# Kernel optimization log

Measured on AMD Instinct MI355X. Metric: run time of the kernel, lower is better.

Reference implementation:

```python
import jax, jax.numpy as jnp
import numpy as np

EPS = 1e-3       # module eps for mask normalization
LN_EPS = 1e-5    # torch LayerNorm default eps


def _layernorm(x, w, b):
    mu = jnp.mean(x, axis=-1, keepdims=True)
    var = jnp.var(x, axis=-1, keepdims=True)
    return (x - mu) * jax.lax.rsqrt(var + LN_EPS) * w + b


def setup_inputs() -> dict:
    key = jax.random.key(0)
    ks = jax.random.split(key, 8)
    N_seq, N_res, c_m, c_h, c_z = 256, 256, 256, 32, 128
    m = jax.random.normal(ks[0], (N_seq, N_res, c_m), jnp.float32)
    mask = jnp.ones((N_seq, N_res), jnp.float32)
    s_m = 1.0 / np.sqrt(c_m)
    ln_w = jnp.ones((c_m,), jnp.float32)
    ln_b = jnp.zeros((c_m,), jnp.float32)
    w1 = jax.random.normal(ks[1], (c_m, c_h), jnp.float32) * s_m
    b1 = jnp.zeros((c_h,), jnp.float32)
    w2 = jax.random.normal(ks[2], (c_m, c_h), jnp.float32) * s_m
    b2 = jnp.zeros((c_h,), jnp.float32)
    # linear_out has init='final' (zeros) in training; use small random so the
    # reference output / gradients are non-trivial for kernel testing.
    w_out = jax.random.normal(ks[3], (c_h * c_h, c_z), jnp.float32) * 0.02
    b_out = jnp.zeros((c_z,), jnp.float32)
    return {"m": m, "mask": mask, "ln_w": ln_w, "ln_b": ln_b,
            "w1": w1, "b1": b1, "w2": w2, "b2": b2,
            "w_out": w_out, "b_out": b_out}


def reference(m, mask, ln_w, ln_b, w1, b1, w2, b2, w_out, b_out):
    # m: [N_seq, N_res, c_m], mask: [N_seq, N_res]
    ln = _layernorm(m, ln_w, ln_b)
    mk = mask[..., None]                                 # [S, N, 1]
    a = (ln @ w1 + b1) * mk                              # [S, N, h]
    b = (ln @ w2 + b2) * mk                              # [S, N, h]
    a = jnp.swapaxes(a, -2, -3)                          # [N, S, h]
    b = jnp.swapaxes(b, -2, -3)                          # [N, S, h]
    # outer product mean over sequences: [N, N, h, h]
    outer = jnp.einsum('isc,jse->ijce', a, b)
    N = outer.shape[0]
    outer = outer.reshape(N, N, -1)                      # [N, N, h*h]
    out = outer @ w_out + b_out                          # [N, N, c_z]
    norm = jnp.einsum('si,sj->ij', mask, mask) + EPS     # [N, N]
    return out / norm[..., None]
```

## Files before the change

kernel.cpp:

```cpp
#include <hip/hip_runtime.h>
#include <hip/hip_bf16.h>
#include <stdint.h>

typedef __bf16 bf16x8 __attribute__((ext_vector_type(8)));
typedef float  f32x4  __attribute__((ext_vector_type(4)));
typedef float  f32x16 __attribute__((ext_vector_type(16)));
typedef __attribute__((address_space(1))) uint32_t u32_g;
typedef __attribute__((address_space(3))) uint32_t u32_l;
typedef unsigned short u16;
typedef u16 u16x4 __attribute__((ext_vector_type(4)));

__device__ __forceinline__ void gload16(const void* g, void* l) {
    __builtin_amdgcn_global_load_lds((u32_g*)g, (u32_l*)l, 16, 0, 0);
}

__device__ __forceinline__ u16 bf16bits(float v) {
    __bf16 h = (__bf16)v;
    return __builtin_bit_cast(u16, h);
}

#define WAITV(n) asm volatile("s_waitcnt vmcnt(" #n ")" ::: "memory")
#define BAR() do { __builtin_amdgcn_s_barrier(); \
                   __builtin_amdgcn_sched_barrier(0); } while (0)

__global__ __launch_bounds__(256) void k_prep(const float* __restrict__ w_out,
                                              const float* __restrict__ mask,
                                              const float* __restrict__ w1,
                                              const float* __restrict__ w2,
                                              u16* __restrict__ WT,
                                              u16* __restrict__ WcatT,
                                              float* __restrict__ rnormv) {
    __shared__ float mcol[256];
    const int b = blockIdx.x, t = threadIdx.x;
    if (b < 512) {
        int idx = b * 256 + t;
        int z = idx >> 10, kc = idx & 1023;
        int c = kc & 31, e = kc >> 5;
        WT[idx] = bf16bits(w_out[(c * 32 + e) * 128 + z]);
    } else if (b < 576) {
        int idx = (b - 512) * 256 + t;
        int n = idx >> 8, k = idx & 255;
        float v = (n < 32) ? w1[k * 32 + n] : w2[k * 32 + (n - 32)];
        WcatT[idx] = bf16bits(v);
    } else {
        int i = b - 576;
        mcol[t] = mask[(size_t)t * 256 + i];
        __syncthreads();
        float acc = 1e-3f;
#pragma unroll 8
        for (int s = 0; s < 256; ++s)
            acc += mcol[s] * mask[(size_t)s * 256 + t];
        rnormv[i * 256 + t] = 1.0f / acc;
    }
}

__global__ __launch_bounds__(256, 2) void k_lnproj(
        const float* __restrict__ M, const float* __restrict__ mask,
        const float* __restrict__ lnw, const float* __restrict__ lnb,
        const float* __restrict__ b1, const float* __restrict__ b2,
        const u16* __restrict__ WcatT,
        u16* __restrict__ AT, u16* __restrict__ BT) {
    __shared__ __align__(16) u16 sh[32768];
    const int tid = threadIdx.x, lane = tid & 63, w = tid >> 6;
    const int i = blockIdx.x, s0 = blockIdx.y * 64;

#pragma unroll
    for (int p = 0; p < 8; ++p) {
        int flat = p * 256 + tid;
        int r = flat >> 5, slot = flat & 31;
        int gs = slot ^ (r & 7);
        const char* src = (const char*)WcatT + (size_t)r * 512 + (size_t)gs * 16;
        char* dst = (char*)sh + 32768 + (size_t)(p * 256 + (tid & ~63)) * 16;
        gload16(src, dst);
    }

    float4 wv = *(const float4*)(lnw + lane * 4);
    float4 bv = *(const float4*)(lnb + lane * 4);
    float4 xv[16];
#pragma unroll
    for (int it = 0; it < 16; ++it) {
        int s = s0 + w * 16 + it;
        xv[it] = *(const float4*)(M + ((size_t)s * 256 + i) * 256 + lane * 4);
    }
#pragma unroll
    for (int it = 0; it < 16; ++it) {
        int row = w * 16 + it;
        float4 x = xv[it];
        float s1 = x.x + x.y + x.z + x.w;
        float s2 = x.x * x.x + x.y * x.y + x.z * x.z + x.w * x.w;
#pragma unroll
        for (int o = 1; o < 64; o <<= 1) {
            s1 += __shfl_xor(s1, o);
            s2 += __shfl_xor(s2, o);
        }
        float mu   = s1 * 0.00390625f;
        float var  = s2 * 0.00390625f - mu * mu;
        float rstd = rsqrtf(var + 1e-5f);
        u16x4 pk;
        pk[0] = bf16bits((x.x - mu) * rstd * wv.x + bv.x);
        pk[1] = bf16bits((x.y - mu) * rstd * wv.y + bv.y);
        pk[2] = bf16bits((x.z - mu) * rstd * wv.z + bv.z);
        pk[3] = bf16bits((x.w - mu) * rstd * wv.w + bv.w);
        int byte = (row * 512 + lane * 8) ^ ((row & 7) << 4);
        *(u16x4*)((char*)sh + byte) = pk;
    }
    __syncthreads();

    f32x4 acc[4] = {};
#pragma unroll
    for (int kk = 0; kk < 8; ++kk) {
        int kb = kk * 64 + ((lane >> 4) << 4);
        int arow = w * 16 + (lane & 15);
        bf16x8 af = *(const bf16x8*)((const char*)sh +
                     ((arow * 512 + kb) ^ ((arow & 7) << 4)));
#pragma unroll
        for (int f = 0; f < 4; ++f) {
            int nrow = f * 16 + (lane & 15);
            bf16x8 bfr = *(const bf16x8*)((const char*)sh + 32768 +
                          ((nrow * 512 + kb) ^ ((nrow & 7) << 4)));
            acc[f] = __builtin_amdgcn_mfma_f32_16x16x32_bf16(af, bfr, acc[f], 0, 0, 0);
        }
    }

    const int sb = s0 + w * 16 + ((lane >> 4) << 2);
    float mk[4];
#pragma unroll
    for (int r = 0; r < 4; ++r) mk[r] = mask[(size_t)(sb + r) * 256 + i];
#pragma unroll
    for (int f = 0; f < 4; ++f) {
        int col = f * 16 + (lane & 15);
        float bias = (col < 32) ? b1[col] : b2[col - 32];
        u16* dst = ((col < 32) ? AT : BT) + ((size_t)i * 32 + (col & 31)) * 256 + sb;
        u16x4 pk;
#pragma unroll
        for (int r = 0; r < 4; ++r)
            pk[r] = bf16bits((acc[f][r] + bias) * mk[r]);
        *(u16x4*)dst = pk;
    }
}

__global__ __launch_bounds__(512, 4) void k_fused(
        const u16* __restrict__ AT, const u16* __restrict__ BT,
        const u16* __restrict__ WT, const float* __restrict__ rnormv,
        const float* __restrict__ b_out, float* __restrict__ out) {
    __shared__ __align__(16) u16 sh[36864];
    const int tid  = threadIdx.x;
    const int lane = tid & 63;
    const int wid  = tid >> 6;
    const int wr   = wid >> 2, wc = wid & 3;
    const int l15  = lane & 15;
    const int q16  = lane >> 4;
    const int lid = blockIdx.x;
    const int x   = lid & 7;
    const int k   = lid >> 3;
    const int bx  = (x & 3) * 16 + (k & 15);
    const int by  = (x >> 2) * 16 + (k >> 4);
    const int m0 = bx * 128, n0 = by * 256;

    f32x4 acc[4][4] = {};

    auto stage = [&](int kt, int buf) {
        char* base = (char*)sh + buf * 24576;
        const int k0 = kt * 32;
        {
            int r = tid >> 2, slot = tid & 3;
            int gs = slot ^ ((r >> 1) & 3);
            gload16((const char*)AT + (((size_t)(m0 + r)) * 256 + k0) * 2 + gs * 16,
                    base + (size_t)(tid & ~63) * 16);
        }
#pragma unroll
        for (int q = 0; q < 2; ++q) {
            int flat = q * 512 + tid;
            int r = flat >> 2, slot = flat & 3;
            int gs = slot ^ ((r >> 1) & 3);
            gload16((const char*)BT + (((size_t)(n0 + r)) * 256 + k0) * 2 + gs * 16,
                    base + 8192 + (size_t)(q * 512 + (tid & ~63)) * 16);
        }
    };

    auto compute = [&](int buf) {
        const char* Ab = (const char*)sh + buf * 24576;
        const char* Bb = Ab + 8192;
        bf16x8 af[4], bfr[4];
#pragma unroll
        for (int mi = 0; mi < 4; ++mi) {
            int rA = wr * 64 + mi * 16 + l15;
            af[mi] = *(const bf16x8*)(Ab + rA * 64 + (q16 ^ ((rA >> 1) & 3)) * 16);
        }
#pragma unroll
        for (int nj = 0; nj < 4; ++nj) {
            int rB = wc * 64 + nj * 16 + l15;
            bfr[nj] = *(const bf16x8*)(Bb + rB * 64 + (q16 ^ ((rB >> 1) & 3)) * 16);
        }
        __builtin_amdgcn_s_setprio(1);
#pragma unroll
        for (int mi = 0; mi < 4; ++mi)
#pragma unroll
            for (int nj = 0; nj < 4; ++nj)
                acc[mi][nj] = __builtin_amdgcn_mfma_f32_16x16x32_bf16(
                    af[mi], bfr[nj], acc[mi][nj], 0, 0, 0);
        __builtin_amdgcn_s_setprio(0);
    };

    stage(0, 0);
    stage(1, 1);
    WAITV(3);
    BAR();
#pragma unroll
    for (int t = 0; t < 8; ++t) {
        if (t + 2 < 8) stage(t + 2, (t + 2) % 3);
        compute(t % 3);
        if (t < 6) { WAITV(3); }
        else if (t == 6) { WAITV(0); }
        BAR();
    }

    const int z0  = (wid & 3) * 32;
    const int hi  = lane >> 5;
    const int p32 = lane & 31;
    const u16* wtrow = WT + (size_t)(z0 + p32) * 1024 + hi * 8;
    const int i0 = bx * 4, j0 = by * 8;
    bf16x8 wbr[8];
    float  rn[16];
    float  bz = 0.f;
    if (wid < 4) {
#pragma unroll
        for (int d = 0; d < 8; ++d)
            wbr[d] = *(const bf16x8*)(wtrow + d * 16);
        bz = b_out[z0 + p32];
#pragma unroll
        for (int r = 0; r < 16; ++r) {
            int pair = (r & 3) + 8 * (r >> 2) + 4 * hi;
            rn[r] = rnormv[(i0 + (pair >> 3)) * 256 + (j0 + (pair & 7))];
        }
    }

#pragma unroll
    for (int mi = 0; mi < 4; ++mi)
#pragma unroll
        for (int nj = 0; nj < 4; ++nj) {
            int m = wr * 64 + mi * 16 + (q16 << 2);
            int n = wc * 64 + nj * 16 + l15;
            int pr = ((m >> 5) << 3) | (n >> 5);
            int c0 = m & 31, e = n & 31;
            int byte = pr * 2048 + (e * 32 + c0) * 2;
            byte ^= ((pr ^ e) & 7) << 4;
            u16x4 pk;
#pragma unroll
            for (int r = 0; r < 4; ++r)
                pk[r] = bf16bits(acc[mi][nj][r]);
            *(u16x4*)((char*)sh + byte) = pk;
        }
    __syncthreads();

    if (wid < 4) {
        f32x16 a0 = {}, a1 = {};

        auto paddr = [&](int ks) {
            int kc = ks * 16 + hi * 8;
            int byte = p32 * 2048 + kc * 2;
            byte ^= ((p32 ^ (kc >> 5)) & 7) << 4;
            return (const bf16x8*)((const char*)sh + byte);
        };
        bf16x8 pa0 = *paddr(0), pa1 = *paddr(1);

#pragma unroll
        for (int ks = 0; ks < 64; ++ks) {
            bf16x8 cur = (ks & 1) ? pa1 : pa0;
            if (ks + 2 < 64) {
                if (ks & 1) pa1 = *paddr(ks + 2);
                else        pa0 = *paddr(ks + 2);
            }
            if (ks & 1)
                a1 = __builtin_amdgcn_mfma_f32_32x32x16_bf16(cur, wbr[ks & 7], a1, 0, 0, 0);
            else
                a0 = __builtin_amdgcn_mfma_f32_32x32x16_bf16(cur, wbr[ks & 7], a0, 0, 0, 0);
            if (ks + 8 < 64)
                wbr[ks & 7] = *(const bf16x8*)(wtrow + (ks + 8) * 16);
        }

        const int z = z0 + p32;
#pragma unroll
        for (int r = 0; r < 16; ++r) {
            int pair = (r & 3) + 8 * (r >> 2) + 4 * hi;
            int i = i0 + (pair >> 3), j = j0 + (pair & 7);
            float val = (a0[r] + a1[r] + bz) * rn[r];
            out[((size_t)(i * 256 + j)) * 128 + z] = val;
        }
    }
}

extern "C" void kernel_launch(void* const* d_in, const int* in_sizes, int n_in,
                              void* d_out, int out_size, void* d_ws, size_t ws_size,
                              hipStream_t stream) {
    const float* M    = (const float*)d_in[0];
    const float* mask = (const float*)d_in[1];
    const float* lnw  = (const float*)d_in[2];
    const float* lnb  = (const float*)d_in[3];
    const float* w1   = (const float*)d_in[4];
    const float* b1   = (const float*)d_in[5];
    const float* w2   = (const float*)d_in[6];
    const float* b2   = (const float*)d_in[7];
    const float* wout = (const float*)d_in[8];
    const float* bout = (const float*)d_in[9];
    float* out = (float*)d_out;

    char* ws = (char*)d_ws;
    u16*   AT    = (u16*)(ws);
    u16*   BT    = (u16*)(ws + 4194304);
    u16*   WT    = (u16*)(ws + 8388608);
    float* rnormv= (float*)(ws + 8650752);
    u16*   WcatT = (u16*)(ws + 8912896);

    k_prep  <<<832, 256, 0, stream>>>(wout, mask, w1, w2, WT, WcatT, rnormv);
    k_lnproj<<<dim3(256, 4), 256, 0, stream>>>(M, mask, lnw, lnb, b1, b2, WcatT, AT, BT);
    k_fused <<<2048, 512, 0, stream>>>(AT, BT, WT, rnormv, bout, out);
}
```

Measured before the change: 121.0 us.

## Load GEMM fragments directly from global memory instead of LDS pipeline

Removes the triple-buffered global_load_lds staging with waitcnt and barriers from the fused kernel's first GEMM. Each wave now reads its bf16x8 A/B fragments straight from global memory into registers, and the shared buffer shrinks. The aim is to drop LDS round-trips and barrier synchronisation. The cost is redundant global or L2 reads across waves, since A rows are shared by the 4 wc waves and B rows by the 2 wr waves, plus exposed load latency with no explicit prefetch.

Result: slower. 206.2 us (+70.5%).

```diff
diff --git a/kernel.cpp b/kernel.cpp
--- a/kernel.cpp
+++ b/kernel.cpp
@@ -18,10 +18,6 @@
     __bf16 h = (__bf16)v;
     return __builtin_bit_cast(u16, h);
 }
-
-#define WAITV(n) asm volatile("s_waitcnt vmcnt(" #n ")" ::: "memory")
-#define BAR() do { __builtin_amdgcn_s_barrier(); \
-                   __builtin_amdgcn_sched_barrier(0); } while (0)
 
 __global__ __launch_bounds__(256) void k_prep(const float* __restrict__ w_out,
                                               const float* __restrict__ mask,
@@ -143,7 +139,7 @@
         const u16* __restrict__ AT, const u16* __restrict__ BT,
         const u16* __restrict__ WT, const float* __restrict__ rnormv,
         const float* __restrict__ b_out, float* __restrict__ out) {
-    __shared__ __align__(16) u16 sh[36864];
+    __shared__ __align__(16) u16 sh[32768];
     const int tid  = threadIdx.x;
     const int lane = tid & 63;
     const int wid  = tid >> 6;
@@ -152,46 +148,25 @@
     const int q16  = lane >> 4;
     const int lid = blockIdx.x;
     const int x   = lid & 7;
-    const int k   = lid >> 3;
-    const int bx  = (x & 3) * 16 + (k & 15);
-    const int by  = (x >> 2) * 16 + (k >> 4);
+    const int kk_ = lid >> 3;
+    const int bx  = (x & 3) * 16 + (kk_ & 15);
+    const int by  = (x >> 2) * 16 + (kk_ >> 4);
     const int m0 = bx * 128, n0 = by * 256;
 
     f32x4 acc[4][4] = {};
 
-    auto stage = [&](int kt, int buf) {
-        char* base = (char*)sh + buf * 24576;
-        const int k0 = kt * 32;
-        {
-            int r = tid >> 2, slot = tid & 3;
-            int gs = slot ^ ((r >> 1) & 3);
-            gload16((const char*)AT + (((size_t)(m0 + r)) * 256 + k0) * 2 + gs * 16,
-                    base + (size_t)(tid & ~63) * 16);
-        }
-#pragma unroll
-        for (int q = 0; q < 2; ++q) {
-            int flat = q * 512 + tid;
-            int r = flat >> 2, slot = flat & 3;
-            int gs = slot ^ ((r >> 1) & 3);
-            gload16((const char*)BT + (((size_t)(n0 + r)) * 256 + k0) * 2 + gs * 16,
-                    base + 8192 + (size_t)(q * 512 + (tid & ~63)) * 16);
-        }
-    };
-
-    auto compute = [&](int buf) {
-        const char* Ab = (const char*)sh + buf * 24576;
-        const char* Bb = Ab + 8192;
+    const u16* Abase = AT + (size_t)(m0 + wr * 64 + l15) * 256 + q16 * 8;
+    const u16* Bbase = BT + (size_t)(n0 + wc * 64 + l15) * 256 + q16 * 8;
+
+#pragma unroll
+    for (int t = 0; t < 8; ++t) {
         bf16x8 af[4], bfr[4];
 #pragma unroll
-        for (int mi = 0; mi < 4; ++mi) {
-            int rA = wr * 64 + mi * 16 + l15;
-            af[mi] = *(const bf16x8*)(Ab + rA * 64 + (q16 ^ ((rA >> 1) & 3)) * 16);
-        }
-#pragma unroll
-        for (int nj = 0; nj < 4; ++nj) {
-            int rB = wc * 64 + nj * 16 + l15;
-            bfr[nj] = *(const bf16x8*)(Bb + rB * 64 + (q16 ^ ((rB >> 1) & 3)) * 16);
-        }
+        for (int mi = 0; mi < 4; ++mi)
+            af[mi] = *(const bf16x8*)(Abase + (size_t)mi * 4096 + t * 32);
+#pragma unroll
+        for (int nj = 0; nj < 4; ++nj)
+            bfr[nj] = *(const bf16x8*)(Bbase + (size_t)nj * 4096 + t * 32);
         __builtin_amdgcn_s_setprio(1);
 #pragma unroll
         for (int mi = 0; mi < 4; ++mi)
@@ -200,19 +175,6 @@
                 acc[mi][nj] = __builtin_amdgcn_mfma_f32_16x16x32_bf16(
                     af[mi], bfr[nj], acc[mi][nj], 0, 0, 0);
         __builtin_amdgcn_s_setprio(0);
-    };
-
-    stage(0, 0);
-    stage(1, 1);
-    WAITV(3);
-    BAR();
-#pragma unroll
-    for (int t = 0; t < 8; ++t) {
-        if (t + 2 < 8) stage(t + 2, (t + 2) % 3);
-        compute(t % 3);
-        if (t < 6) { WAITV(3); }
-        else if (t == 6) { WAITV(0); }
-        BAR();
     }
 
     const int z0  = (wid & 3) * 32;
```
